# Kernel tuning notes

Hardware: AMD Instinct MI355X
Metric: run time of the kernel (lower is better)

## Reference

```python
import jax, jax.numpy as jnp
import numpy as np

N_NODES = 50000


def _gcn_layer(x, src, dst, W, b, n_nodes):
    # x: [N, Cin] -> linear -> [N, Cout]
    h = x @ W.T + b
    # degree over destination (col) index, including self loops
    deg = jax.ops.segment_sum(jnp.ones(src.shape[0], dtype=x.dtype), dst,
                              num_segments=n_nodes)
    dinv = jnp.where(deg > 0, deg ** -0.5, jnp.zeros((), x.dtype))
    norm = dinv[src] * dinv[dst]                      # [E]
    msg = h[src] * norm[:, None]                      # gather + scale
    return jax.ops.segment_sum(msg, dst, num_segments=n_nodes)  # scatter-add


def setup_inputs() -> dict:
    key = jax.random.key(0)
    k1, k2, k3, k4, k5, k6 = jax.random.split(key, 6)
    num_features = 128
    hidden_dim = 128
    n_edges = 1_600_000
    x = jax.random.normal(k1, (N_NODES, num_features), dtype=jnp.float32)
    edge_index = jax.random.randint(k2, (2, n_edges), 0, N_NODES, dtype=jnp.int64)
    bound1 = 1.0 / np.sqrt(num_features)
    W1 = jax.random.uniform(k3, (hidden_dim, num_features), jnp.float32, -bound1, bound1)
    b1 = jax.random.uniform(k4, (hidden_dim,), jnp.float32, -bound1, bound1)
    bound2 = 1.0 / np.sqrt(hidden_dim)
    W2 = jax.random.uniform(k5, (hidden_dim, hidden_dim), jnp.float32, -bound2, bound2)
    b2 = jax.random.uniform(k6, (hidden_dim,), jnp.float32, -bound2, bound2)
    return {"x": x, "edge_index": edge_index, "W1": W1, "b1": b1, "W2": W2, "b2": b2}


def reference(x, edge_index, W1, b1, W2, b2):
    n_nodes = x.shape[0]
    # add_self_loops: append (i, i) for every node
    loops = jnp.arange(n_nodes, dtype=edge_index.dtype)
    src = jnp.concatenate([edge_index[0], loops])
    dst = jnp.concatenate([edge_index[1], loops])
    h = _gcn_layer(x, src, dst, W1, b1, n_nodes)
    h = jax.nn.relu(h)
    # dropout is identity in eval mode (deterministic reference)
    out = _gcn_layer(h, src, dst, W2, b2, n_nodes)
    return out
```

## Files before the change

kernel.cpp:

```cpp
#include <hip/hip_runtime.h>


static constexpr int F = 128;
static constexpr int NR = 128;
static constexpr int CH = 4096;
static constexpr int RMAX = 512;

__device__ __forceinline__ unsigned f2b(float x) {
  unsigned u = __float_as_uint(x);
  return (u + 0x7fffu + ((u >> 16) & 1u)) >> 16;
}
__device__ __forceinline__ float b_lo(unsigned u) {
  return __uint_as_float(u << 16);
}
__device__ __forceinline__ float b_hi(unsigned u) {
  return __uint_as_float(u & 0xffff0000u);
}

__global__ void k_zero_i32(int* __restrict__ p, int n) {
  int i = blockIdx.x * blockDim.x + threadIdx.x;
  if (i < n) p[i] = 0;
}

__global__ __launch_bounds__(256) void k_hist(const int* __restrict__ dst,
                                              int E, int R,
                                              int* __restrict__ rtot) {
  __shared__ int h[RMAX];
  for (int i = threadIdx.x; i < R; i += 256) h[i] = 0;
  __syncthreads();
  const int e0 = blockIdx.x * CH;
  const int e1 = min(e0 + CH, E);
  for (int i = e0 + threadIdx.x; i < e1; i += 256)
    atomicAdd(&h[dst[i] >> 7], 1);
  __syncthreads();
  for (int i = threadIdx.x; i < R; i += 256)
    if (h[i]) atomicAdd(&rtot[i], h[i]);
}

__global__ __launch_bounds__(512) void k_scanR(const int* __restrict__ rtot,
                                               int R, int E,
                                               int* __restrict__ rbase,
                                               int* __restrict__ gcur) {
  __shared__ int s[512];
  const int t = threadIdx.x;
  const int v = (t < R) ? rtot[t] : 0;
  s[t] = v;
  __syncthreads();
#pragma unroll
  for (int off = 1; off < 512; off <<= 1) {
    int a = (t >= off) ? s[t - off] : 0;
    __syncthreads();
    s[t] += a;
    __syncthreads();
  }
  if (t < R) {
    const int b = s[t] - v;
    rbase[t] = b;
    gcur[t] = b;
  }
  if (t == 0) rbase[R] = E;
}

__global__ __launch_bounds__(256) void k_part(const int* __restrict__ src,
                                              const int* __restrict__ dst,
                                              int E, int R,
                                              int* __restrict__ gcur,
                                              unsigned* __restrict__ rsorted) {
  __shared__ int h[RMAX];
  __shared__ int cur[RMAX];
  for (int i = threadIdx.x; i < R; i += 256) h[i] = 0;
  __syncthreads();
  const int e0 = blockIdx.x * CH;
  const int e1 = min(e0 + CH, E);
  for (int i = e0 + threadIdx.x; i < e1; i += 256)
    atomicAdd(&h[dst[i] >> 7], 1);
  __syncthreads();
  for (int i = threadIdx.x; i < R; i += 256)
    cur[i] = h[i] ? atomicAdd(&gcur[i], h[i]) : 0;
  __syncthreads();
  for (int i = e0 + threadIdx.x; i < e1; i += 256) {
    const int d = dst[i];
    const int s = src[i];
    const int pos = atomicAdd(&cur[d >> 7], 1);
    rsorted[pos] = ((unsigned)(d & (NR - 1)) << 16) | (unsigned)s;
  }
}

__global__ __launch_bounds__(256) void k_fillR(
    const unsigned* __restrict__ rsorted, const int* __restrict__ rbase,
    int N, int E, int* __restrict__ rowptr, float* __restrict__ dinv,
    int* __restrict__ csr) {
  __shared__ int cnt[NR];
  __shared__ int sc[NR];
  __shared__ int cur[NR];
  const int r = blockIdx.x;
  const int tid = threadIdx.x;
  const int b = rbase[r];
  const int e = rbase[r + 1];
  if (tid < NR) cnt[tid] = 0;
  __syncthreads();
  for (int i = b + tid; i < e; i += 256)
    atomicAdd(&cnt[rsorted[i] >> 16], 1);
  __syncthreads();
  if (tid < NR) sc[tid] = cnt[tid];
  __syncthreads();
#pragma unroll
  for (int off = 1; off < NR; off <<= 1) {
    int a = (tid < NR && tid >= off) ? sc[tid - off] : 0;
    __syncthreads();
    if (tid < NR) sc[tid] += a;
    __syncthreads();
  }
  if (tid < NR) {
    const int excl = sc[tid] - cnt[tid];
    cur[tid] = excl;
    const int node = r * NR + tid;
    if (node < N) {
      rowptr[node] = b + excl;
      dinv[node] = rsqrtf((float)(cnt[tid] + 1));
    }
  }
  if (r == 0 && tid == 0) rowptr[N] = E;
  __syncthreads();
  for (int i = b + tid; i < e; i += 256) {
    const unsigned v = rsorted[i];
    const int pos = b + atomicAdd(&cur[v >> 16], 1);
    csr[pos] = (int)(v & 0xFFFFu);
  }
}

static constexpr int ASTR = 68;
static constexpr int BSTR = 132;

__global__ __launch_bounds__(256) void k_gemm(
    const float* __restrict__ A, const float* __restrict__ W,
    const float* __restrict__ bias, const float* __restrict__ dinv,
    uint2* __restrict__ hout, int n) {
  __shared__ float As[32][ASTR];
  __shared__ float Bs[32][BSTR];
  const int tid = threadIdx.x;
  const int tm = tid >> 5;
  const int tn = tid & 31;
  const int m0 = blockIdx.x * 64;

  float acc[8][4];
#pragma unroll
  for (int i = 0; i < 8; ++i)
#pragma unroll
    for (int j = 0; j < 4; ++j) acc[i][j] = 0.f;

  for (int kt = 0; kt < F; kt += 32) {
    __syncthreads();
#pragma unroll
    for (int l = 0; l < 2; ++l) {
      const int idx = tid + l * 256;
      const int r = idx >> 3;
      const int j = idx & 7;
      const int grow = m0 + r;
      float4 v = make_float4(0.f, 0.f, 0.f, 0.f);
      if (grow < n) v = *(const float4*)(A + (size_t)grow * F + kt + j * 4);
      As[j * 4 + 0][r] = v.x;
      As[j * 4 + 1][r] = v.y;
      As[j * 4 + 2][r] = v.z;
      As[j * 4 + 3][r] = v.w;
    }
#pragma unroll
    for (int l = 0; l < 4; ++l) {
      const int idx = tid + l * 256;
      const int r = idx >> 3;
      const int j = idx & 7;
      const float4 v = *(const float4*)(W + (size_t)r * F + kt + j * 4);
      Bs[j * 4 + 0][r] = v.x;
      Bs[j * 4 + 1][r] = v.y;
      Bs[j * 4 + 2][r] = v.z;
      Bs[j * 4 + 3][r] = v.w;
    }
    __syncthreads();
#pragma unroll
    for (int k = 0; k < 32; ++k) {
      const float4 a0 = *(const float4*)&As[k][tm * 8];
      const float4 a1 = *(const float4*)&As[k][tm * 8 + 4];
      const float4 b = *(const float4*)&Bs[k][tn * 4];
      acc[0][0] += a0.x * b.x; acc[0][1] += a0.x * b.y; acc[0][2] += a0.x * b.z; acc[0][3] += a0.x * b.w;
      acc[1][0] += a0.y * b.x; acc[1][1] += a0.y * b.y; acc[1][2] += a0.y * b.z; acc[1][3] += a0.y * b.w;
      acc[2][0] += a0.z * b.x; acc[2][1] += a0.z * b.y; acc[2][2] += a0.z * b.z; acc[2][3] += a0.z * b.w;
      acc[3][0] += a0.w * b.x; acc[3][1] += a0.w * b.y; acc[3][2] += a0.w * b.z; acc[3][3] += a0.w * b.w;
      acc[4][0] += a1.x * b.x; acc[4][1] += a1.x * b.y; acc[4][2] += a1.x * b.z; acc[4][3] += a1.x * b.w;
      acc[5][0] += a1.y * b.x; acc[5][1] += a1.y * b.y; acc[5][2] += a1.y * b.z; acc[5][3] += a1.y * b.w;
      acc[6][0] += a1.z * b.x; acc[6][1] += a1.z * b.y; acc[6][2] += a1.z * b.z; acc[6][3] += a1.z * b.w;
      acc[7][0] += a1.w * b.x; acc[7][1] += a1.w * b.y; acc[7][2] += a1.w * b.z; acc[7][3] += a1.w * b.w;
    }
  }

  const float4 bv = *(const float4*)(bias + tn * 4);
#pragma unroll
  for (int i = 0; i < 8; ++i) {
    const int grow = m0 + tm * 8 + i;
    if (grow < n) {
      const float dv = dinv[grow];
      const float ox = (acc[i][0] + bv.x) * dv;
      const float oy = (acc[i][1] + bv.y) * dv;
      const float oz = (acc[i][2] + bv.z) * dv;
      const float ow = (acc[i][3] + bv.w) * dv;
      uint2 p;
      p.x = f2b(ox) | (f2b(oy) << 16);
      p.y = f2b(oz) | (f2b(ow) << 16);
      hout[(size_t)grow * 32 + tn] = p;
    }
  }
}

template <bool RELU>
__global__ __launch_bounds__(256) void k_pull(
    const int* __restrict__ rowptr, const int* __restrict__ csr,
    const uint2* __restrict__ h, const float* __restrict__ dinv,
    float* __restrict__ out, int n) {
  const int wid = (blockIdx.x * blockDim.x + threadIdx.x) >> 6;
  if (wid >= n) return;
  const int lane = threadIdx.x & 63;
  const int half = lane >> 5;
  const int l32 = lane & 31;
  const int beg = rowptr[wid];
  const int end = rowptr[wid + 1];

  float4 acc = make_float4(0.f, 0.f, 0.f, 0.f);
  if (half == 0) {
    const uint2 u = h[(size_t)wid * 32 + l32];
    acc.x = b_lo(u.x); acc.y = b_hi(u.x);
    acc.z = b_lo(u.y); acc.w = b_hi(u.y);
  }

  int k = beg + half;
  for (; k + 6 < end; k += 8) {
    const int s0 = csr[k];
    const int s1 = csr[k + 2];
    const int s2 = csr[k + 4];
    const int s3 = csr[k + 6];
    const uint2 u0 = h[(size_t)s0 * 32 + l32];
    const uint2 u1 = h[(size_t)s1 * 32 + l32];
    const uint2 u2 = h[(size_t)s2 * 32 + l32];
    const uint2 u3 = h[(size_t)s3 * 32 + l32];
    acc.x += b_lo(u0.x) + b_lo(u1.x) + b_lo(u2.x) + b_lo(u3.x);
    acc.y += b_hi(u0.x) + b_hi(u1.x) + b_hi(u2.x) + b_hi(u3.x);
    acc.z += b_lo(u0.y) + b_lo(u1.y) + b_lo(u2.y) + b_lo(u3.y);
    acc.w += b_hi(u0.y) + b_hi(u1.y) + b_hi(u2.y) + b_hi(u3.y);
  }
  for (; k < end; k += 2) {
    const uint2 u = h[(size_t)csr[k] * 32 + l32];
    acc.x += b_lo(u.x);
    acc.y += b_hi(u.x);
    acc.z += b_lo(u.y);
    acc.w += b_hi(u.y);
  }

  acc.x += __shfl_xor(acc.x, 32, 64);
  acc.y += __shfl_xor(acc.y, 32, 64);
  acc.z += __shfl_xor(acc.z, 32, 64);
  acc.w += __shfl_xor(acc.w, 32, 64);

  if (half == 0) {
    const float dv = dinv[wid];
    float4 r;
    r.x = acc.x * dv;
    r.y = acc.y * dv;
    r.z = acc.z * dv;
    r.w = acc.w * dv;
    if (RELU) {
      r.x = fmaxf(r.x, 0.f);
      r.y = fmaxf(r.y, 0.f);
      r.z = fmaxf(r.z, 0.f);
      r.w = fmaxf(r.w, 0.f);
    }
    ((float4*)out)[(size_t)wid * 32 + l32] = r;
  }
}

extern "C" void kernel_launch(void* const* d_in, const int* in_sizes, int n_in,
                              void* d_out, int out_size, void* d_ws, size_t ws_size,
                              hipStream_t stream) {
  const float* x  = (const float*)d_in[0];
  const int*   ei = (const int*)d_in[1];
  const float* W1 = (const float*)d_in[2];
  const float* b1 = (const float*)d_in[3];
  const float* W2 = (const float*)d_in[4];
  const float* b2 = (const float*)d_in[5];

  const int N = in_sizes[0] / F;
  const int E = in_sizes[1] / 2;
  const int* src = ei;
  const int* dst = ei + E;
  const int R = (N + NR - 1) / NR;
  const int C = (E + CH - 1) / CH;

  char* ws = (char*)d_ws;
  int*      rtot    = (int*)(ws);
  int*      rbase   = (int*)(ws + (4u << 10));
  int*      gcur    = (int*)(ws + (8u << 10));
  float*    dinv    = (float*)(ws + (16u << 10));
  int*      rowptr  = (int*)(ws + (256u << 10));
  unsigned* rsorted = (unsigned*)(ws + (1u << 20));
  int*      csr     = (int*)(ws + (8u << 20));
  uint2*    hbuf    = (uint2*)(ws + (16u << 20));
  float*    out     = (float*)d_out;

  const int B = 256;
  const int gemmBlocks = (N + 63) / 64;
  const int pullBlocks = (N * 64 + B - 1) / B;

  k_zero_i32<<<1, 512, 0, stream>>>(rtot, R);
  k_hist<<<C, B, 0, stream>>>(dst, E, R, rtot);
  k_scanR<<<1, 512, 0, stream>>>(rtot, R, E, rbase, gcur);
  k_part<<<C, B, 0, stream>>>(src, dst, E, R, gcur, rsorted);
  k_fillR<<<R, B, 0, stream>>>(rsorted, rbase, N, E, rowptr, dinv, csr);

  k_gemm<<<gemmBlocks, B, 0, stream>>>(x, W1, b1, dinv, hbuf, N);
  k_pull<true><<<pullBlocks, B, 0, stream>>>(rowptr, csr, hbuf, dinv, out, N);

  k_gemm<<<gemmBlocks, B, 0, stream>>>(out, W2, b2, dinv, hbuf, N);
  k_pull<false><<<pullBlocks, B, 0, stream>>>(rowptr, csr, hbuf, dinv, out, N);
}
```

Before: 231.1 us.

## Replace FP32 SIMT GEMM with split-bf16 MFMA GEMM

Replaces the shared-memory FP32 FMA GEMM with a matrix-core version using 16x16x32 bf16 MFMA. Both operands are split into hi and lo bf16 parts and three MFMAs (hi*hi, hi*lo, lo*hi) recover near-FP32 accuracy. The weights are pre-split by a small new kernel, activations are split in registers, and shared memory is no longer used. The cost is extra launches and global reads of W per wave. Output stores are now scattered 16-bit writes instead of packed 64-bit writes.

```diff
diff --git a/kernel.cpp b/kernel.cpp
--- a/kernel.cpp
+++ b/kernel.cpp
@@ -5,6 +5,10 @@
 static constexpr int NR = 128;
 static constexpr int CH = 4096;
 static constexpr int RMAX = 512;
+
+typedef __attribute__((ext_vector_type(8))) short bf16x8;
+typedef __attribute__((ext_vector_type(4))) float f32x4;
+typedef __attribute__((ext_vector_type(4))) unsigned short u16x4;
 
 __device__ __forceinline__ unsigned f2b(float x) {
   unsigned u = __float_as_uint(x);
@@ -129,83 +133,85 @@
   }
 }
 
-static constexpr int ASTR = 68;
-static constexpr int BSTR = 132;
-
-__global__ __launch_bounds__(256) void k_gemm(
-    const float* __restrict__ A, const float* __restrict__ W,
-    const float* __restrict__ bias, const float* __restrict__ dinv,
-    uint2* __restrict__ hout, int n) {
-  __shared__ float As[32][ASTR];
-  __shared__ float Bs[32][BSTR];
-  const int tid = threadIdx.x;
-  const int tm = tid >> 5;
-  const int tn = tid & 31;
-  const int m0 = blockIdx.x * 64;
-
-  float acc[8][4];
-#pragma unroll
-  for (int i = 0; i < 8; ++i)
-#pragma unroll
-    for (int j = 0; j < 4; ++j) acc[i][j] = 0.f;
-
+__global__ __launch_bounds__(256) void k_splitW(const float* __restrict__ W,
+                                                unsigned short* __restrict__ hi,
+                                                unsigned short* __restrict__ lo) {
+  const int i = blockIdx.x * 256 + threadIdx.x;
+  const float x = W[i];
+  const unsigned h = f2b(x);
+  hi[i] = (unsigned short)h;
+  lo[i] = (unsigned short)f2b(x - __uint_as_float(h << 16));
+}
+
+__global__ __launch_bounds__(256) void k_gemm_mfma(
+    const float* __restrict__ A, const unsigned short* __restrict__ Whi,
+    const unsigned short* __restrict__ Wlo, const float* __restrict__ bias,
+    const float* __restrict__ dinv, unsigned short* __restrict__ hout, int n) {
+  const int wid = threadIdx.x >> 6;
+  const int lane = threadIdx.x & 63;
+  const int r = lane & 15;
+  const int g = lane >> 4;
+  const int m0 = blockIdx.x * 64 + wid * 16;
+  const int arow = m0 + r;
+
+  f32x4 acc[8];
+#pragma unroll
+  for (int f = 0; f < 8; ++f) acc[f] = (f32x4){0.f, 0.f, 0.f, 0.f};
+
+#pragma unroll
   for (int kt = 0; kt < F; kt += 32) {
-    __syncthreads();
-#pragma unroll
-    for (int l = 0; l < 2; ++l) {
-      const int idx = tid + l * 256;
-      const int r = idx >> 3;
-      const int j = idx & 7;
-      const int grow = m0 + r;
-      float4 v = make_float4(0.f, 0.f, 0.f, 0.f);
-      if (grow < n) v = *(const float4*)(A + (size_t)grow * F + kt + j * 4);
-      As[j * 4 + 0][r] = v.x;
-      As[j * 4 + 1][r] = v.y;
-      As[j * 4 + 2][r] = v.z;
-      As[j * 4 + 3][r] = v.w;
-    }
-#pragma unroll
-    for (int l = 0; l < 4; ++l) {
-      const int idx = tid + l * 256;
-      const int r = idx >> 3;
-      const int j = idx & 7;
-      const float4 v = *(const float4*)(W + (size_t)r * F + kt + j * 4);
-      Bs[j * 4 + 0][r] = v.x;
-      Bs[j * 4 + 1][r] = v.y;
-      Bs[j * 4 + 2][r] = v.z;
-      Bs[j * 4 + 3][r] = v.w;
-    }
-    __syncthreads();
-#pragma unroll
-    for (int k = 0; k < 32; ++k) {
-      const float4 a0 = *(const float4*)&As[k][tm * 8];
-      const float4 a1 = *(const float4*)&As[k][tm * 8 + 4];
-      const float4 b = *(const float4*)&Bs[k][tn * 4];
-      acc[0][0] += a0.x * b.x; acc[0][1] += a0.x * b.y; acc[0][2] += a0.x * b.z; acc[0][3] += a0.x * b.w;
-      acc[1][0] += a0.y * b.x; acc[1][1] += a0.y * b.y; acc[1][2] += a0.y * b.z; acc[1][3] += a0.y * b.w;
-      acc[2][0] += a0.z * b.x; acc[2][1] += a0.z * b.y; acc[2][2] += a0.z * b.z; acc[2][3] += a0.z * b.w;
-      acc[3][0] += a0.w * b.x; acc[3][1] += a0.w * b.y; acc[3][2] += a0.w * b.z; acc[3][3] += a0.w * b.w;
-      acc[4][0] += a1.x * b.x; acc[4][1] += a1.x * b.y; acc[4][2] += a1.x * b.z; acc[4][3] += a1.x * b.w;
-      acc[5][0] += a1.y * b.x; acc[5][1] += a1.y * b.y; acc[5][2] += a1.y * b.z; acc[5][3] += a1.y * b.w;
-      acc[6][0] += a1.z * b.x; acc[6][1] += a1.z * b.y; acc[6][2] += a1.z * b.z; acc[6][3] += a1.z * b.w;
-      acc[7][0] += a1.w * b.x; acc[7][1] += a1.w * b.y; acc[7][2] += a1.w * b.z; acc[7][3] += a1.w * b.w;
-    }
-  }
-
-  const float4 bv = *(const float4*)(bias + tn * 4);
-#pragma unroll
-  for (int i = 0; i < 8; ++i) {
-    const int grow = m0 + tm * 8 + i;
-    if (grow < n) {
-      const float dv = dinv[grow];
-      const float ox = (acc[i][0] + bv.x) * dv;
-      const float oy = (acc[i][1] + bv.y) * dv;
-      const float oz = (acc[i][2] + bv.z) * dv;
-      const float ow = (acc[i][3] + bv.w) * dv;
-      uint2 p;
-      p.x = f2b(ox) | (f2b(oy) << 16);
-      p.y = f2b(oz) | (f2b(ow) << 16);
-      hout[(size_t)grow * 32 + tn] = p;
+    float4 a0 = make_float4(0.f, 0.f, 0.f, 0.f);
+    float4 a1 = make_float4(0.f, 0.f, 0.f, 0.f);
+    if (arow < n) {
+      a0 = *(const float4*)(A + (size_t)arow * F + kt + 4 * g);
+      a1 = *(const float4*)(A + (size_t)arow * F + kt + 16 + 4 * g);
+    }
+    bf16x8 ahi, alo;
+    {
+      unsigned h;
+      h = f2b(a0.x); ahi[0] = (short)h; alo[0] = (short)f2b(a0.x - __uint_as_float(h << 16));
+      h = f2b(a0.y); ahi[1] = (short)h; alo[1] = (short)f2b(a0.y - __uint_as_float(h << 16));
+      h = f2b(a0.z); ahi[2] = (short)h; alo[2] = (short)f2b(a0.z - __uint_as_float(h << 16));
+      h = f2b(a0.w); ahi[3] = (short)h; alo[3] = (short)f2b(a0.w - __uint_as_float(h << 16));
+      h = f2b(a1.x); ahi[4] = (short)h; alo[4] = (short)f2b(a1.x - __uint_as_float(h << 16));
+      h = f2b(a1.y); ahi[5] = (short)h; alo[5] = (short)f2b(a1.y - __uint_as_float(h << 16));
+      h = f2b(a1.z); ahi[6] = (short)h; alo[6] = (short)f2b(a1.z - __uint_as_float(h << 16));
+      h = f2b(a1.w); ahi[7] = (short)h; alo[7] = (short)f2b(a1.w - __uint_as_float(h << 16));
+    }
+#pragma unroll
+    for (int f = 0; f < 8; ++f) {
+      const int col = f * 16 + r;
+      const size_t wb = (size_t)col * F + kt + 4 * g;
+      const u16x4 h0 = *(const u16x4*)(Whi + wb);
+      const u16x4 h1 = *(const u16x4*)(Whi + wb + 16);
+      const u16x4 l0 = *(const u16x4*)(Wlo + wb);
+      const u16x4 l1 = *(const u16x4*)(Wlo + wb + 16);
+      bf16x8 bhi, blo;
+      bhi[0] = (short)h0[0]; bhi[1] = (short)h0[1]; bhi[2] = (short)h0[2]; bhi[3] = (short)h0[3];
+      bhi[4] = (short)h1[0]; bhi[5] = (short)h1[1]; bhi[6] = (short)h1[2]; bhi[7] = (short)h1[3];
+      blo[0] = (short)l0[0]; blo[1] = (short)l0[1]; blo[2] = (short)l0[2]; blo[3] = (short)l0[3];
+      blo[4] = (short)l1[0]; blo[5] = (short)l1[1]; blo[6] = (short)l1[2]; blo[7] = (short)l1[3];
+      acc[f] = __builtin_amdgcn_mfma_f32_16x16x32_bf16(ahi, bhi, acc[f], 0, 0, 0);
+      acc[f] = __builtin_amdgcn_mfma_f32_16x16x32_bf16(ahi, blo, acc[f], 0, 0, 0);
+      acc[f] = __builtin_amdgcn_mfma_f32_16x16x32_bf16(alo, bhi, acc[f], 0, 0, 0);
+    }
+  }
+
+  int orow[4];
+  float dv[4];
+#pragma unroll
+  for (int j = 0; j < 4; ++j) {
+    orow[j] = m0 + 4 * g + j;
+    dv[j] = (orow[j] < n) ? dinv[orow[j]] : 0.f;
+  }
+#pragma unroll
+  for (int f = 0; f < 8; ++f) {
+    const int col = f * 16 + r;
+    const float bv = bias[col];
+#pragma unroll
+    for (int j = 0; j < 4; ++j) {
+      if (orow[j] < n)
+        hout[(size_t)orow[j] * F + col] = (unsigned short)f2b((acc[f][j] + bv) * dv[j]);
     }
   }
 }
@@ -293,29 +299,35 @@
   const int C = (E + CH - 1) / CH;
 
   char* ws = (char*)d_ws;
-  int*      rtot    = (int*)(ws);
-  int*      rbase   = (int*)(ws + (4u << 10));
-  int*      gcur    = (int*)(ws + (8u << 10));
-  float*    dinv    = (float*)(ws + (16u << 10));
-  int*      rowptr  = (int*)(ws + (256u << 10));
-  unsigned* rsorted = (unsigned*)(ws + (1u << 20));
-  int*      csr     = (int*)(ws + (8u << 20));
-  uint2*    hbuf    = (uint2*)(ws + (16u << 20));
-  float*    out     = (float*)d_out;
+  int*            rtot    = (int*)(ws);
+  int*            rbase   = (int*)(ws + (4u << 10));
+  int*            gcur    = (int*)(ws + (8u << 10));
+  float*          dinv    = (float*)(ws + (16u << 10));
+  int*            rowptr  = (int*)(ws + (256u << 10));
+  unsigned short* Whi1    = (unsigned short*)(ws + (480u << 10));
+  unsigned short* Wlo1    = (unsigned short*)(ws + (512u << 10));
+  unsigned short* Whi2    = (unsigned short*)(ws + (544u << 10));
+  unsigned short* Wlo2    = (unsigned short*)(ws + (576u << 10));
+  unsigned*       rsorted = (unsigned*)(ws + (1u << 20));
+  int*            csr     = (int*)(ws + (8u << 20));
+  unsigned short* hbuf    = (unsigned short*)(ws + (16u << 20));
+  float*          out     = (float*)d_out;
 
   const int B = 256;
   const int gemmBlocks = (N + 63) / 64;
   const int pullBlocks = (N * 64 + B - 1) / B;
 
-  k_zero_i32<<<1, 512, 0, stream>>>(rtot, R);
+  k_zero_i32<<<(R + 255) / 256, B, 0, stream>>>(rtot, R);
   k_hist<<<C, B, 0, stream>>>(dst, E, R, rtot);
   k_scanR<<<1, 512, 0, stream>>>(rtot, R, E, rbase, gcur);
   k_part<<<C, B, 0, stream>>>(src, dst, E, R, gcur, rsorted);
   k_fillR<<<R, B, 0, stream>>>(rsorted, rbase, N, E, rowptr, dinv, csr);
-
-  k_gemm<<<gemmBlocks, B, 0, stream>>>(x, W1, b1, dinv, hbuf, N);
-  k_pull<true><<<pullBlocks, B, 0, stream>>>(rowptr, csr, hbuf, dinv, out, N);
-
-  k_gemm<<<gemmBlocks, B, 0, stream>>>(out, W2, b2, dinv, hbuf, N);
-  k_pull<false><<<pullBlocks, B, 0, stream>>>(rowptr, csr, hbuf, dinv, out, N);
-}
+  k_splitW<<<64, B, 0, stream>>>(W1, Whi1, Wlo1);
+  k_splitW<<<64, B, 0, stream>>>(W2, Whi2, Wlo2);
+
+  k_gemm_mfma<<<gemmBlocks, B, 0, stream>>>(x, Whi1, Wlo1, b1, dinv, hbuf, N);
+  k_pull<true><<<pullBlocks, B, 0, stream>>>(rowptr, csr, (const uint2*)hbuf, dinv, out, N);
+
+  k_gemm_mfma<<<gemmBlocks, B, 0, stream>>>(out, Whi2, Wlo2, b2, dinv, hbuf, N);
+  k_pull<false><<<pullBlocks, B, 0, stream>>>(rowptr, csr, (const uint2*)hbuf, dinv, out, N);
+}
```

Result: slower. 301.1 us (+30.3%).
